# Kernel optimization log

Hardware: AMD Instinct MI355X
Metric: run time of the kernel (lower is better)

The kernel has to match this reference:

```python
import jax, jax.numpy as jnp
import numpy as np

HIDDEN = 1024
HEADS = 16
HEAD = HIDDEN // HEADS


def setup_inputs() -> dict:
    key = jax.random.key(0)
    ks = jax.random.split(key, 10)
    B, T, N = 4, 1024, 1024
    x = jax.random.normal(ks[0], (B, T, HIDDEN), dtype=jnp.float32)
    encoder_feature = jax.random.normal(ks[1], (B, N, HIDDEN), dtype=jnp.float32)
    s = 1.0 / np.sqrt(HIDDEN)
    Wq = jax.random.normal(ks[2], (HIDDEN, HIDDEN), dtype=jnp.float32) * s
    bq = jax.random.normal(ks[3], (HIDDEN,), dtype=jnp.float32) * 0.02
    Wk = jax.random.normal(ks[4], (HIDDEN, HIDDEN), dtype=jnp.float32) * s
    bk = jax.random.normal(ks[5], (HIDDEN,), dtype=jnp.float32) * 0.02
    Wv = jax.random.normal(ks[6], (HIDDEN, HIDDEN), dtype=jnp.float32) * s
    bv = jax.random.normal(ks[7], (HIDDEN,), dtype=jnp.float32) * 0.02
    return {"x": x, "encoder_feature": encoder_feature,
            "Wq": Wq, "bq": bq, "Wk": Wk, "bk": bk, "Wv": Wv, "bv": bv}


def reference(x, encoder_feature, Wq, bq, Wk, bk, Wv, bv):
    B, T, _ = x.shape
    N = encoder_feature.shape[1]
    # torch Linear: y = x @ W.T + b
    q = (x @ Wq.T + bq).reshape(B, T, HEADS, HEAD)
    k = (encoder_feature @ Wk.T + bk).reshape(B, N, HEADS, HEAD)
    v = (encoder_feature @ Wv.T + bv).reshape(B, N, HEADS, HEAD)
    att = jnp.einsum('bthd,bnhd->bhtn', q, k) / jnp.sqrt(jnp.float32(HEAD))
    # causal tril mask sliced to (T, N): position t attends to n <= t
    mask = jnp.tril(jnp.ones((T, N), dtype=bool))
    att = jnp.where(mask[None, None], att, jnp.finfo(att.dtype).min)
    att = jax.nn.softmax(att, axis=-1)
    out = jnp.einsum('bhtn,bnhd->bthd', att, v).reshape(B, T, HIDDEN)
    # NOTE: original forward never applies out_proj; dropout=0.0 (identity)
    return out
```

## Files before the change

kernel.cpp:

```cpp
#include <hip/hip_runtime.h>
#include <hip/hip_bf16.h>
#include <cstdint>
#include <cstddef>

#define B_SZ 4
#define T_SZ 1024
#define N_SZ 1024
#define HID 1024
#define NHEADS 16
#define DHEAD 64

typedef __bf16 bf16x8 __attribute__((ext_vector_type(8)));
typedef __bf16 bf16x4 __attribute__((ext_vector_type(4)));
typedef float floatx4 __attribute__((ext_vector_type(4)));

#define LDT 72
#define LKV 72
#define LP  72

#define SM_SCALE_LOG2E 0.18033688011112042f

__device__ __forceinline__ void async_copy16(const void* gsrc, void* ldst) {
    __builtin_amdgcn_global_load_lds(
        (const __attribute__((address_space(1))) void*)(uintptr_t)gsrc,
        (__attribute__((address_space(3))) void*)(uintptr_t)ldst, 16, 0, 0);
}

__global__ __launch_bounds__(256)
void cvt5_f32_bf16(const float* __restrict__ x, const float* __restrict__ enc,
                   const float* __restrict__ wq, const float* __restrict__ wk,
                   const float* __restrict__ wv,
                   __bf16* __restrict__ xb, __bf16* __restrict__ eb,
                   __bf16* __restrict__ wqb, __bf16* __restrict__ wkb,
                   __bf16* __restrict__ wvb)
{
#pragma unroll
    for (int c = 0; c < 8; ++c) {
        const int chunk = blockIdx.x * 8 + c;
        const float* s; __bf16* d; int base;
        if (chunk < 2048)      { s = x;   d = xb;  base = chunk; }
        else if (chunk < 4096) { s = enc; d = eb;  base = chunk - 2048; }
        else if (chunk < 4608) { s = wq;  d = wqb; base = chunk - 4096; }
        else if (chunk < 5120) { s = wk;  d = wkb; base = chunk - 4608; }
        else                   { s = wv;  d = wvb; base = chunk - 5120; }
        const size_t off = (size_t)base * 2048 + (size_t)threadIdx.x * 8;
        const float4 a = *(const float4*)(s + off);
        const float4 b = *(const float4*)(s + off + 4);
        bf16x8 o;
        o[0] = (__bf16)a.x; o[1] = (__bf16)a.y; o[2] = (__bf16)a.z; o[3] = (__bf16)a.w;
        o[4] = (__bf16)b.x; o[5] = (__bf16)b.y; o[6] = (__bf16)b.z; o[7] = (__bf16)b.w;
        *(bf16x8*)(d + off) = o;
    }
}

#define PBAR() do {                              \
    asm volatile("" ::: "memory");               \
    __builtin_amdgcn_s_barrier();                \
    __builtin_amdgcn_sched_barrier(0);           \
} while (0)

#define MFMA_Q(QM, QN, BREG) do {                                             \
    __builtin_amdgcn_s_setprio(1);                                            \
    _Pragma("unroll")                                                         \
    for (int mf_ = 0; mf_ < 4; ++mf_) {                                       \
        _Pragma("unroll")                                                     \
        for (int nf_ = 0; nf_ < 2; ++nf_) {                                   \
            acc[QM][QN][mf_][nf_] = __builtin_amdgcn_mfma_f32_16x16x32_bf16(  \
                a[mf_][0], BREG[nf_][0], acc[QM][QN][mf_][nf_], 0, 0, 0);     \
            acc[QM][QN][mf_][nf_] = __builtin_amdgcn_mfma_f32_16x16x32_bf16(  \
                a[mf_][1], BREG[nf_][1], acc[QM][QN][mf_][nf_], 0, 0, 0);     \
        }                                                                     \
    }                                                                         \
    __builtin_amdgcn_s_setprio(0);                                            \
} while (0)

#define LOAD_A(BUF, HALF) do {                                                \
    _Pragma("unroll")                                                         \
    for (int mf_ = 0; mf_ < 4; ++mf_) {                                       \
        a[mf_][0] = ldsA(BUF, HALF, mf_, 0);                                  \
        a[mf_][1] = ldsA(BUF, HALF, mf_, 1);                                  \
    }                                                                         \
} while (0)

#define LOAD_B(DST, BUF, HALF) do {                                           \
    _Pragma("unroll")                                                         \
    for (int nf_ = 0; nf_ < 2; ++nf_) {                                       \
        DST[nf_][0] = ldsB(BUF, HALF, nf_, 0);                                \
        DST[nf_][1] = ldsB(BUF, HALF, nf_, 1);                                \
    }                                                                         \
} while (0)

__global__ __launch_bounds__(512, 2)
void gemm3_256_8ph(const __bf16* __restrict__ xb, const __bf16* __restrict__ eb,
                   const __bf16* __restrict__ wqb, const __bf16* __restrict__ wkb,
                   const __bf16* __restrict__ wvb,
                   const float* __restrict__ bq, const float* __restrict__ bk,
                   const float* __restrict__ bv,
                   __bf16* __restrict__ qo, __bf16* __restrict__ ko,
                   __bf16* __restrict__ vo)
{
    __shared__ __align__(16) __bf16 AS[2][2][8192];
    __shared__ __align__(16) __bf16 BS[2][2][8192];

    const int bid = blockIdx.x;
    const int swz = (bid & 7) * 24 + (bid >> 3);
    const int mt  = swz >> 2;
    const int nt  = swz & 3;
    const int z   = mt >> 4;
    const int bm  = (mt & 15) << 8;
    const int bn  = nt << 8;

    const __bf16* A; const __bf16* W; const float* bias; __bf16* C;
    if (z == 0)      { A = xb; W = wqb; bias = bq; C = qo; }
    else if (z == 1) { A = eb; W = wkb; bias = bk; C = ko; }
    else             { A = eb; W = wvb; bias = bv; C = vo; }

    const int tid  = threadIdx.x;
    const int lane = tid & 63;
    const int wid  = tid >> 6;
    const int l15  = lane & 15;
    const int quad = lane >> 4;
    const int wmid = wid >> 2;
    const int wnid = wid & 3;

    const int sr  = tid >> 3;
    const int sch = tid & 7;

    auto stage2 = [&](const __bf16* src, __bf16* dst, int gRow0, int kt) {
        const int c = (sch ^ (sr & 7)) << 3;
        async_copy16(src + (size_t)(gRow0 + sr) * HID + kt * 64 + c,
                     (char*)dst + tid * 16);
        async_copy16(src + (size_t)(gRow0 + sr + 64) * HID + kt * 64 + c,
                     (char*)dst + 8192 + tid * 16);
    };

    auto ldsA = [&](int buf, int half, int mf, int kk) -> bf16x8 {
        const int r = wmid * 64 + mf * 16 + l15;
        return *(const bf16x8*)((const char*)&AS[buf][half][0] + r * 128 +
                                (((kk * 4 + quad) ^ (r & 7)) << 4));
    };
    auto ldsB = [&](int buf, int half, int nf, int kk) -> bf16x8 {
        const int r = wnid * 32 + nf * 16 + l15;
        return *(const bf16x8*)((const char*)&BS[buf][half][0] + r * 128 +
                                (((kk * 4 + quad) ^ (r & 7)) << 4));
    };

    bf16x8 a[4][2], b0[2][2], b1[2][2];
    floatx4 acc[2][2][4][2];
#pragma unroll
    for (int i = 0; i < 2; ++i)
#pragma unroll
        for (int j = 0; j < 2; ++j)
#pragma unroll
            for (int m = 0; m < 4; ++m)
#pragma unroll
                for (int n = 0; n < 2; ++n)
                    acc[i][j][m][n] = (floatx4)(0.0f);

    stage2(A, &AS[0][0][0], bm,       0);
    stage2(W, &BS[0][0][0], bn,       0);
    stage2(W, &BS[0][1][0], bn + 128, 0);
    stage2(A, &AS[0][1][0], bm + 128, 0);
    stage2(A, &AS[1][0][0], bm,       1);
    stage2(W, &BS[1][0][0], bn,       1);
    stage2(W, &BS[1][1][0], bn + 128, 1);
    asm volatile("s_waitcnt vmcnt(6)" ::: "memory");
    PBAR();

#pragma unroll 1
    for (int it = 0; it < 8; ++it) {
        const int kt1 = 2 * it + 1;
        const int kta = (it < 7) ? 2 * it + 2 : 14;
        const int ktb = (it < 7) ? 2 * it + 3 : 15;

        LOAD_A(0, 0);
        LOAD_B(b0, 0, 0);
        stage2(A, &AS[1][1][0], bm + 128, kt1);
        PBAR();
        MFMA_Q(0, 0, b0);
        PBAR();
        LOAD_B(b1, 0, 1);
        stage2(A, &AS[0][0][0], bm, kta);
        PBAR();
        MFMA_Q(0, 1, b1);
        PBAR();
        LOAD_A(0, 1);
        stage2(W, &BS[0][0][0], bn, kta);
        PBAR();
        MFMA_Q(1, 1, b1);
        PBAR();
        stage2(W, &BS[0][1][0], bn + 128, kta);
        PBAR();
        MFMA_Q(1, 0, b0);
        asm volatile("s_waitcnt vmcnt(6)" ::: "memory");
        PBAR();
        LOAD_A(1, 0);
        LOAD_B(b0, 1, 0);
        stage2(A, &AS[0][1][0], bm + 128, kta);
        PBAR();
        MFMA_Q(0, 0, b0);
        PBAR();
        LOAD_B(b1, 1, 1);
        stage2(A, &AS[1][0][0], bm, ktb);
        PBAR();
        MFMA_Q(0, 1, b1);
        PBAR();
        LOAD_A(1, 1);
        stage2(W, &BS[1][0][0], bn, ktb);
        PBAR();
        MFMA_Q(1, 1, b1);
        PBAR();
        stage2(W, &BS[1][1][0], bn + 128, ktb);
        PBAR();
        MFMA_Q(1, 0, b0);
        asm volatile("s_waitcnt vmcnt(6)" ::: "memory");
        PBAR();
    }

#pragma unroll
    for (int qn = 0; qn < 2; ++qn)
#pragma unroll
        for (int nf = 0; nf < 2; ++nf) {
            const int n = bn + qn * 128 + wnid * 32 + nf * 16 + l15;
            const float bias_f = bias[n];
#pragma unroll
            for (int qm = 0; qm < 2; ++qm)
#pragma unroll
                for (int mf = 0; mf < 4; ++mf) {
                    const int m0 = bm + qm * 128 + wmid * 64 + mf * 16 + quad * 4;
#pragma unroll
                    for (int r = 0; r < 4; ++r)
                        C[(size_t)(m0 + r) * HID + n] =
                            (__bf16)(acc[qm][qn][mf][nf][r] + bias_f);
                }
        }
}

#undef LOAD_A
#undef LOAD_B
#undef MFMA_Q
#undef PBAR

__global__ __launch_bounds__(256)
void gemm_bt_bias_f32in(const float* __restrict__ A,
                        const float* __restrict__ W,
                        const float* __restrict__ bias,
                        __hip_bfloat16* __restrict__ C)
{
    constexpr int K = HID;
    __shared__ __align__(16) __hip_bfloat16 As[128 * LDT];
    __shared__ __align__(16) __hip_bfloat16 Bs[128 * LDT];

    const int tid  = threadIdx.x;
    const int wave = tid >> 6;
    const int lane = tid & 63;
    const int bm = blockIdx.y * 128;
    const int bn = blockIdx.x * 128;
    const int wm = (wave >> 1) * 64;
    const int wn = (wave & 1) * 64;

    floatx4 acc[4][4];
#pragma unroll
    for (int i = 0; i < 4; ++i)
#pragma unroll
        for (int j = 0; j < 4; ++j)
            acc[i][j] = (floatx4)(0.0f);

    const int lr = tid >> 4;
    const int lc = (tid & 15) * 4;

    for (int k0 = 0; k0 < K; k0 += 64) {
#pragma unroll
        for (int qq = 0; qq < 8; ++qq) {
            const int r = lr + qq * 16;
            const float4 a4 = *(const float4*)(A + (size_t)(bm + r) * K + k0 + lc);
            const float4 w4 = *(const float4*)(W + (size_t)(bn + r) * K + k0 + lc);
            bf16x4 av, wv;
            av[0] = (__bf16)a4.x; av[1] = (__bf16)a4.y; av[2] = (__bf16)a4.z; av[3] = (__bf16)a4.w;
            wv[0] = (__bf16)w4.x; wv[1] = (__bf16)w4.y; wv[2] = (__bf16)w4.z; wv[3] = (__bf16)w4.w;
            *(bf16x4*)(As + r * LDT + lc) = av;
            *(bf16x4*)(Bs + r * LDT + lc) = wv;
        }
        __syncthreads();
#pragma unroll
        for (int kk = 0; kk < 2; ++kk) {
            const int krow = kk * 32 + (lane >> 4) * 8;
            const int mrow = wm + (lane & 15);
            const int nrow = wn + (lane & 15);
            bf16x8 af[4], bfr[4];
#pragma unroll
            for (int i = 0; i < 4; ++i) {
                af[i]  = *(const bf16x8*)(As + (mrow + i * 16) * LDT + krow);
                bfr[i] = *(const bf16x8*)(Bs + (nrow + i * 16) * LDT + krow);
            }
#pragma unroll
            for (int mi = 0; mi < 4; ++mi)
#pragma unroll
                for (int ni = 0; ni < 4; ++ni)
                    acc[mi][ni] = __builtin_amdgcn_mfma_f32_16x16x32_bf16(
                        af[mi], bfr[ni], acc[mi][ni], 0, 0, 0);
        }
        __syncthreads();
    }

    const int crow0 = bm + wm + (lane >> 4) * 4;
    const int ccol0 = bn + wn + (lane & 15);
#pragma unroll
    for (int ni = 0; ni < 4; ++ni) {
        const int n = ccol0 + ni * 16;
        const float bias_f = bias[n];
#pragma unroll
        for (int mi = 0; mi < 4; ++mi) {
#pragma unroll
            for (int r = 0; r < 4; ++r) {
                const int m = crow0 + mi * 16 + r;
                C[(size_t)m * HID + n] = __float2bfloat16(acc[mi][ni][r] + bias_f);
            }
        }
    }
}

__global__ __launch_bounds__(256)
void attn_flash_mfma_v4(const __bf16* __restrict__ q,
                        const __bf16* __restrict__ k,
                        const __bf16* __restrict__ v,
                        float* __restrict__ out)
{
    __shared__ __align__(16) __bf16 Ks[2][64 * LKV];
    __shared__ __align__(16) __bf16 Vt[2][64 * LKV];
    __shared__ __align__(16) __bf16 Ps[4][32 * LP];

    const int tid  = threadIdx.x;
    const int wave = tid >> 6;
    const int lane = tid & 63;
    const int l15  = lane & 15;
    const int quad = lane >> 4;

    const int bx = blockIdx.x;
    const int jj = bx & 7;
    const int bt = ((bx >> 8) & 1) ? jj : 7 - jj;
    const int bh = bx >> 3;
    const int h  = bh & (NHEADS - 1);
    const int b  = bh >> 4;
    const int t0 = bt * 128;

    const __bf16* kbase = k + (size_t)b * N_SZ * HID + h * DHEAD;
    const __bf16* vbase = v + (size_t)b * N_SZ * HID + h * DHEAD;

    bf16x8 qf[2][2];
    {
        const __bf16* qb = q + (size_t)(b * T_SZ + t0 + wave * 32) * HID + h * DHEAD;
#pragma unroll
        for (int g = 0; g < 2; ++g)
#pragma unroll
            for (int kk = 0; kk < 2; ++kk) {
                const bf16x8 raw = *(const bf16x8*)(qb + (size_t)(g * 16 + l15) * HID
                                                    + kk * 32 + quad * 8);
#pragma unroll
                for (int j = 0; j < 8; ++j)
                    qf[g][kk][j] = (__bf16)((float)raw[j] * SM_SCALE_LOG2E);
            }
    }

    const int kr = tid >> 3;
    const int kc = (tid & 7) * 8;
    const int vn = tid & 63;
    const int vd = (tid >> 6) * 8;

#pragma unroll
    for (int p = 0; p < 2; ++p) {
        *(bf16x8*)(&Ks[0][(kr + p * 32) * LKV + kc]) =
            *(const bf16x8*)(kbase + (size_t)(kr + p * 32) * HID + kc);
        const bf16x8 vv = *(const bf16x8*)(vbase + (size_t)vn * HID + vd + p * 32);
#pragma unroll
        for (int j = 0; j < 8; ++j)
            Vt[0][(vd + p * 32 + j) * LKV + vn] = vv[j];
    }
    __syncthreads();

    float lsum[2] = {0.f, 0.f};
    floatx4 oacc[2][4];
#pragma unroll
    for (int g = 0; g < 2; ++g)
#pragma unroll
        for (int nd = 0; nd < 4; ++nd) oacc[g][nd] = (floatx4)(0.0f);

    __bf16* pw = &Ps[wave][0];
    const int ntiles = 2 * bt + 2;

    for (int it = 0; it < ntiles; ++it) {
        const int bi = it & 1;
        const int n0 = it * 64;

        bf16x8 nk0, nk1, nv0, nv1;
        const bool pf = (it + 1 < ntiles);
        if (pf) {
            const int nn0 = n0 + 64;
            nk0 = *(const bf16x8*)(kbase + (size_t)(nn0 + kr) * HID + kc);
            nk1 = *(const bf16x8*)(kbase + (size_t)(nn0 + kr + 32) * HID + kc);
            nv0 = *(const bf16x8*)(vbase + (size_t)(nn0 + vn) * HID + vd);
            nv1 = *(const bf16x8*)(vbase + (size_t)(nn0 + vn) * HID + vd + 32);
        }

        floatx4 st[2][4];
#pragma unroll
        for (int g = 0; g < 2; ++g)
#pragma unroll
            for (int ni = 0; ni < 4; ++ni) st[g][ni] = (floatx4)(0.0f);
        const __bf16* ksb = &Ks[bi][0];
#pragma unroll
        for (int kk = 0; kk < 2; ++kk) {
            const int ko = kk * 32 + quad * 8;
#pragma unroll
            for (int ni = 0; ni < 4; ++ni) {
                const bf16x8 af = *(const bf16x8*)(ksb + (ni * 16 + l15) * LKV + ko);
                st[0][ni] = __builtin_amdgcn_mfma_f32_16x16x32_bf16(af, qf[0][kk], st[0][ni], 0, 0, 0);
                st[1][ni] = __builtin_amdgcn_mfma_f32_16x16x32_bf16(af, qf[1][kk], st[1][ni], 0, 0, 0);
            }
        }

        const bool msk = (it >= 2 * bt);
#pragma unroll
        for (int g = 0; g < 2; ++g) {
            const int tq = t0 + wave * 32 + g * 16 + l15;
#pragma unroll
            for (int ni = 0; ni < 4; ++ni) {
                bf16x4 pk;
#pragma unroll
                for (int r = 0; r < 4; ++r) {
                    float p = exp2f(st[g][ni][r]);
                    if (msk) {
                        const int nn = n0 + ni * 16 + quad * 4 + r;
                        p = (nn > tq) ? 0.f : p;
                    }
                    lsum[g] += p;
                    pk[r] = (__bf16)p;
                }
                *(bf16x4*)(pw + (g * 16 + l15) * LP + ni * 16 + quad * 4) = pk;
            }
        }

        const __bf16* vtb = &Vt[bi][0];
#pragma unroll
        for (int kk = 0; kk < 2; ++kk) {
            const int ko = kk * 32 + quad * 8;
            const bf16x8 bp0 = *(const bf16x8*)(pw + l15 * LP + ko);
            const bf16x8 bp1 = *(const bf16x8*)(pw + (16 + l15) * LP + ko);
#pragma unroll
            for (int nd = 0; nd < 4; ++nd) {
                const bf16x8 av = *(const bf16x8*)(vtb + (nd * 16 + l15) * LKV + ko);
                oacc[0][nd] = __builtin_amdgcn_mfma_f32_16x16x32_bf16(av, bp0, oacc[0][nd], 0, 0, 0);
                oacc[1][nd] = __builtin_amdgcn_mfma_f32_16x16x32_bf16(av, bp1, oacc[1][nd], 0, 0, 0);
            }
        }

        if (pf) {
            const int wb = bi ^ 1;
            *(bf16x8*)(&Ks[wb][kr * LKV + kc]) = nk0;
            *(bf16x8*)(&Ks[wb][(kr + 32) * LKV + kc]) = nk1;
#pragma unroll
            for (int j = 0; j < 8; ++j) {
                Vt[wb][(vd + j) * LKV + vn] = nv0[j];
                Vt[wb][(vd + 32 + j) * LKV + vn] = nv1[j];
            }
        }
        __syncthreads();
    }

#pragma unroll
    for (int g = 0; g < 2; ++g) {
        lsum[g] += __shfl_xor(lsum[g], 16, 64);
        lsum[g] += __shfl_xor(lsum[g], 32, 64);
    }
#pragma unroll
    for (int g = 0; g < 2; ++g) {
        const float invl = 1.0f / lsum[g];
        const int trow = t0 + wave * 32 + g * 16 + l15;
        float* ob = out + (size_t)(b * T_SZ + trow) * HID + h * DHEAD + quad * 4;
#pragma unroll
        for (int nd = 0; nd < 4; ++nd) {
            float4 o4;
            o4.x = oacc[g][nd][0] * invl;
            o4.y = oacc[g][nd][1] * invl;
            o4.z = oacc[g][nd][2] * invl;
            o4.w = oacc[g][nd][3] * invl;
            *(float4*)(ob + nd * 16) = o4;
        }
    }
}

extern "C" void kernel_launch(void* const* d_in, const int* in_sizes, int n_in,
                              void* d_out, int out_size, void* d_ws, size_t ws_size,
                              hipStream_t stream) {
    const float* x   = (const float*)d_in[0];
    const float* enc = (const float*)d_in[1];
    const float* Wq  = (const float*)d_in[2];
    const float* bq  = (const float*)d_in[3];
    const float* Wk  = (const float*)d_in[4];
    const float* bk  = (const float*)d_in[5];
    const float* Wv  = (const float*)d_in[6];
    const float* bv  = (const float*)d_in[7];
    float* out = (float*)d_out;

    char* ws = (char*)d_ws;
    const size_t MiB = 1024 * 1024;
    __bf16* q_ws = (__bf16*)(ws);
    __bf16* k_ws = (__bf16*)(ws + 8 * MiB);
    __bf16* v_ws = (__bf16*)(ws + 16 * MiB);

    const dim3 blk(256);
    if (ws_size >= 46 * MiB) {
        __bf16* xb  = (__bf16*)(ws + 24 * MiB);
        __bf16* eb  = (__bf16*)(ws + 32 * MiB);
        __bf16* wqb = (__bf16*)(ws + 40 * MiB);
        __bf16* wkb = (__bf16*)(ws + 42 * MiB);
        __bf16* wvb = (__bf16*)(ws + 44 * MiB);
        cvt5_f32_bf16<<<dim3(704), blk, 0, stream>>>(x, enc, Wq, Wk, Wv,
                                                     xb, eb, wqb, wkb, wvb);
        gemm3_256_8ph<<<dim3(192), dim3(512), 0, stream>>>(
            xb, eb, wqb, wkb, wvb, bq, bk, bv, q_ws, k_ws, v_ws);
    } else {
        const dim3 gg(HID / 128, (B_SZ * T_SZ) / 128);
        gemm_bt_bias_f32in<<<gg, blk, 0, stream>>>(x,   Wq, bq, (__hip_bfloat16*)q_ws);
        gemm_bt_bias_f32in<<<gg, blk, 0, stream>>>(enc, Wk, bk, (__hip_bfloat16*)k_ws);
        gemm_bt_bias_f32in<<<gg, blk, 0, stream>>>(enc, Wv, bv, (__hip_bfloat16*)v_ws);
    }

    attn_flash_mfma_v4<<<dim3(512), blk, 0, stream>>>(q_ws, k_ws, v_ws, out);
}
```

Measured before the change: 160.8 us.

## Halve attention query tile, swizzle LDS layouts, add MFMA priority hints

```diff
diff --git a/kernel.cpp b/kernel.cpp
--- a/kernel.cpp
+++ b/kernel.cpp
@@ -12,13 +12,14 @@
 
 typedef __bf16 bf16x8 __attribute__((ext_vector_type(8)));
 typedef __bf16 bf16x4 __attribute__((ext_vector_type(4)));
+typedef __bf16 bf16x2 __attribute__((ext_vector_type(2)));
 typedef float floatx4 __attribute__((ext_vector_type(4)));
 
 #define LDT 72
-#define LKV 72
-#define LP  72
 
 #define SM_SCALE_LOG2E 0.18033688011112042f
+
+#define SWZ(row, colbyte) (((row) << 7) + ((((colbyte) + (((row) & 7) << 4))) & 127))
 
 __device__ __forceinline__ void async_copy16(const void* gsrc, void* ldst) {
     __builtin_amdgcn_global_load_lds(
@@ -320,15 +321,15 @@
     }
 }
 
-__global__ __launch_bounds__(256)
-void attn_flash_mfma_v4(const __bf16* __restrict__ q,
+__global__ __launch_bounds__(256, 4)
+void attn_flash_mfma_v5(const __bf16* __restrict__ q,
                         const __bf16* __restrict__ k,
                         const __bf16* __restrict__ v,
                         float* __restrict__ out)
 {
-    __shared__ __align__(16) __bf16 Ks[2][64 * LKV];
-    __shared__ __align__(16) __bf16 Vt[2][64 * LKV];
-    __shared__ __align__(16) __bf16 Ps[4][32 * LP];
+    __shared__ __align__(16) char Ks[2][64 * 128];
+    __shared__ __align__(16) char Vt[2][64 * 128];
+    __shared__ __align__(16) char Ps[4][16 * 128];
 
     const int tid  = threadIdx.x;
     const int wave = tid >> 6;
@@ -337,153 +338,144 @@
     const int quad = lane >> 4;
 
     const int bx = blockIdx.x;
-    const int jj = bx & 7;
-    const int bt = ((bx >> 8) & 1) ? jj : 7 - jj;
-    const int bh = bx >> 3;
+    const int jj = bx & 15;
+    const int bt = ((bx >> 8) & 1) ? jj : 15 - jj;
+    const int bh = bx >> 4;
     const int h  = bh & (NHEADS - 1);
     const int b  = bh >> 4;
-    const int t0 = bt * 128;
+    const int t0 = bt * 64;
 
     const __bf16* kbase = k + (size_t)b * N_SZ * HID + h * DHEAD;
     const __bf16* vbase = v + (size_t)b * N_SZ * HID + h * DHEAD;
 
-    bf16x8 qf[2][2];
+    bf16x8 qf[2];
     {
-        const __bf16* qb = q + (size_t)(b * T_SZ + t0 + wave * 32) * HID + h * DHEAD;
-#pragma unroll
-        for (int g = 0; g < 2; ++g)
-#pragma unroll
-            for (int kk = 0; kk < 2; ++kk) {
-                const bf16x8 raw = *(const bf16x8*)(qb + (size_t)(g * 16 + l15) * HID
-                                                    + kk * 32 + quad * 8);
-#pragma unroll
-                for (int j = 0; j < 8; ++j)
-                    qf[g][kk][j] = (__bf16)((float)raw[j] * SM_SCALE_LOG2E);
-            }
-    }
-
-    const int kr = tid >> 3;
-    const int kc = (tid & 7) * 8;
-    const int vn = tid & 63;
-    const int vd = (tid >> 6) * 8;
-
-#pragma unroll
-    for (int p = 0; p < 2; ++p) {
-        *(bf16x8*)(&Ks[0][(kr + p * 32) * LKV + kc]) =
-            *(const bf16x8*)(kbase + (size_t)(kr + p * 32) * HID + kc);
-        const bf16x8 vv = *(const bf16x8*)(vbase + (size_t)vn * HID + vd + p * 32);
-#pragma unroll
-        for (int j = 0; j < 8; ++j)
-            Vt[0][(vd + p * 32 + j) * LKV + vn] = vv[j];
+        const __bf16* qb = q + (size_t)(b * T_SZ + t0 + wave * 16 + l15) * HID + h * DHEAD;
+#pragma unroll
+        for (int kk = 0; kk < 2; ++kk) {
+            const bf16x8 raw = *(const bf16x8*)(qb + kk * 32 + quad * 8);
+#pragma unroll
+            for (int j = 0; j < 8; ++j)
+                qf[kk][j] = (__bf16)((float)raw[j] * SM_SCALE_LOG2E);
+        }
+    }
+
+    const int kr  = tid >> 3;
+    const int kce = (tid & 7) * 8;
+    const int vn2 = (tid & 31) * 2;
+    const int vd2 = (tid >> 5) * 8;
+
+    {
+        *(bf16x8*)(&Ks[0][0] + SWZ(kr, kce * 2)) =
+            *(const bf16x8*)(kbase + (size_t)kr * HID + kce);
+        *(bf16x8*)(&Ks[0][0] + SWZ(kr + 32, kce * 2)) =
+            *(const bf16x8*)(kbase + (size_t)(kr + 32) * HID + kce);
+        const bf16x8 va = *(const bf16x8*)(vbase + (size_t)vn2 * HID + vd2);
+        const bf16x8 vb = *(const bf16x8*)(vbase + (size_t)(vn2 + 1) * HID + vd2);
+#pragma unroll
+        for (int j = 0; j < 8; ++j) {
+            bf16x2 t2; t2[0] = va[j]; t2[1] = vb[j];
+            *(bf16x2*)(&Vt[0][0] + SWZ(vd2 + j, vn2 * 2)) = t2;
+        }
     }
     __syncthreads();
 
-    float lsum[2] = {0.f, 0.f};
-    floatx4 oacc[2][4];
-#pragma unroll
-    for (int g = 0; g < 2; ++g)
-#pragma unroll
-        for (int nd = 0; nd < 4; ++nd) oacc[g][nd] = (floatx4)(0.0f);
-
-    __bf16* pw = &Ps[wave][0];
-    const int ntiles = 2 * bt + 2;
+    float lsum = 0.f;
+    floatx4 oacc[4];
+#pragma unroll
+    for (int nd = 0; nd < 4; ++nd) oacc[nd] = (floatx4)(0.0f);
+
+    char* pw = &Ps[wave][0];
+    const int ntiles = bt + 1;
+    const int tq = t0 + wave * 16 + l15;
 
     for (int it = 0; it < ntiles; ++it) {
         const int bi = it & 1;
         const int n0 = it * 64;
 
-        bf16x8 nk0, nk1, nv0, nv1;
+        bf16x8 nk0, nk1, nva, nvb;
         const bool pf = (it + 1 < ntiles);
         if (pf) {
             const int nn0 = n0 + 64;
-            nk0 = *(const bf16x8*)(kbase + (size_t)(nn0 + kr) * HID + kc);
-            nk1 = *(const bf16x8*)(kbase + (size_t)(nn0 + kr + 32) * HID + kc);
-            nv0 = *(const bf16x8*)(vbase + (size_t)(nn0 + vn) * HID + vd);
-            nv1 = *(const bf16x8*)(vbase + (size_t)(nn0 + vn) * HID + vd + 32);
-        }
-
-        floatx4 st[2][4];
-#pragma unroll
-        for (int g = 0; g < 2; ++g)
-#pragma unroll
-            for (int ni = 0; ni < 4; ++ni) st[g][ni] = (floatx4)(0.0f);
-        const __bf16* ksb = &Ks[bi][0];
+            nk0 = *(const bf16x8*)(kbase + (size_t)(nn0 + kr) * HID + kce);
+            nk1 = *(const bf16x8*)(kbase + (size_t)(nn0 + kr + 32) * HID + kce);
+            nva = *(const bf16x8*)(vbase + (size_t)(nn0 + vn2) * HID + vd2);
+            nvb = *(const bf16x8*)(vbase + (size_t)(nn0 + vn2 + 1) * HID + vd2);
+        }
+
+        floatx4 st[4];
+#pragma unroll
+        for (int ni = 0; ni < 4; ++ni) st[ni] = (floatx4)(0.0f);
+        const char* ksb = &Ks[bi][0];
+        __builtin_amdgcn_s_setprio(1);
 #pragma unroll
         for (int kk = 0; kk < 2; ++kk) {
-            const int ko = kk * 32 + quad * 8;
+            const int cb = kk * 64 + quad * 16;
 #pragma unroll
             for (int ni = 0; ni < 4; ++ni) {
-                const bf16x8 af = *(const bf16x8*)(ksb + (ni * 16 + l15) * LKV + ko);
-                st[0][ni] = __builtin_amdgcn_mfma_f32_16x16x32_bf16(af, qf[0][kk], st[0][ni], 0, 0, 0);
-                st[1][ni] = __builtin_amdgcn_mfma_f32_16x16x32_bf16(af, qf[1][kk], st[1][ni], 0, 0, 0);
+                const bf16x8 af = *(const bf16x8*)(ksb + SWZ(ni * 16 + l15, cb));
+                st[ni] = __builtin_amdgcn_mfma_f32_16x16x32_bf16(af, qf[kk], st[ni], 0, 0, 0);
             }
         }
-
-        const bool msk = (it >= 2 * bt);
-#pragma unroll
-        for (int g = 0; g < 2; ++g) {
-            const int tq = t0 + wave * 32 + g * 16 + l15;
-#pragma unroll
-            for (int ni = 0; ni < 4; ++ni) {
-                bf16x4 pk;
-#pragma unroll
-                for (int r = 0; r < 4; ++r) {
-                    float p = exp2f(st[g][ni][r]);
-                    if (msk) {
-                        const int nn = n0 + ni * 16 + quad * 4 + r;
-                        p = (nn > tq) ? 0.f : p;
-                    }
-                    lsum[g] += p;
-                    pk[r] = (__bf16)p;
+        __builtin_amdgcn_s_setprio(0);
+
+        const bool msk = (it == bt);
+#pragma unroll
+        for (int ni = 0; ni < 4; ++ni) {
+            bf16x4 pk;
+#pragma unroll
+            for (int r = 0; r < 4; ++r) {
+                float p = exp2f(st[ni][r]);
+                if (msk) {
+                    const int nn = n0 + ni * 16 + quad * 4 + r;
+                    p = (nn > tq) ? 0.f : p;
                 }
-                *(bf16x4*)(pw + (g * 16 + l15) * LP + ni * 16 + quad * 4) = pk;
+                lsum += p;
+                pk[r] = (__bf16)p;
             }
-        }
-
-        const __bf16* vtb = &Vt[bi][0];
+            *(bf16x4*)(pw + SWZ(l15, ni * 32 + quad * 8)) = pk;
+        }
+
+        const char* vtb = &Vt[bi][0];
+        __builtin_amdgcn_s_setprio(1);
 #pragma unroll
         for (int kk = 0; kk < 2; ++kk) {
-            const int ko = kk * 32 + quad * 8;
-            const bf16x8 bp0 = *(const bf16x8*)(pw + l15 * LP + ko);
-            const bf16x8 bp1 = *(const bf16x8*)(pw + (16 + l15) * LP + ko);
+            const int cb = kk * 64 + quad * 16;
+            const bf16x8 bp = *(const bf16x8*)(pw + SWZ(l15, cb));
 #pragma unroll
             for (int nd = 0; nd < 4; ++nd) {
-                const bf16x8 av = *(const bf16x8*)(vtb + (nd * 16 + l15) * LKV + ko);
-                oacc[0][nd] = __builtin_amdgcn_mfma_f32_16x16x32_bf16(av, bp0, oacc[0][nd], 0, 0, 0);
-                oacc[1][nd] = __builtin_amdgcn_mfma_f32_16x16x32_bf16(av, bp1, oacc[1][nd], 0, 0, 0);
+                const bf16x8 av = *(const bf16x8*)(vtb + SWZ(nd * 16 + l15, cb));
+                oacc[nd] = __builtin_amdgcn_mfma_f32_16x16x32_bf16(av, bp, oacc[nd], 0, 0, 0);
             }
         }
+        __builtin_amdgcn_s_setprio(0);
 
         if (pf) {
-            const int wb = bi ^ 1;
-            *(bf16x8*)(&Ks[wb][kr * LKV + kc]) = nk0;
-            *(bf16x8*)(&Ks[wb][(kr + 32) * LKV + kc]) = nk1;
+            char* kd = &Ks[bi ^ 1][0];
+            char* vd = &Vt[bi ^ 1][0];
+            *(bf16x8*)(kd + SWZ(kr, kce * 2)) = nk0;
+            *(bf16x8*)(kd + SWZ(kr + 32, kce * 2)) = nk1;
 #pragma unroll
             for (int j = 0; j < 8; ++j) {
-                Vt[wb][(vd + j) * LKV + vn] = nv0[j];
-                Vt[wb][(vd + 32 + j) * LKV + vn] = nv1[j];
+                bf16x2 t2; t2[0] = nva[j]; t2[1] = nvb[j];
+                *(bf16x2*)(vd + SWZ(vd2 + j, vn2 * 2)) = t2;
             }
         }
         __syncthreads();
     }
 
-#pragma unroll
-    for (int g = 0; g < 2; ++g) {
-        lsum[g] += __shfl_xor(lsum[g], 16, 64);
-        lsum[g] += __shfl_xor(lsum[g], 32, 64);
-    }
-#pragma unroll
-    for (int g = 0; g < 2; ++g) {
-        const float invl = 1.0f / lsum[g];
-        const int trow = t0 + wave * 32 + g * 16 + l15;
-        float* ob = out + (size_t)(b * T_SZ + trow) * HID + h * DHEAD + quad * 4;
+    lsum += __shfl_xor(lsum, 16, 64);
+    lsum += __shfl_xor(lsum, 32, 64);
+    {
+        const float invl = 1.0f / lsum;
+        float* ob = out + (size_t)(b * T_SZ + tq) * HID + h * DHEAD + quad * 4;
 #pragma unroll
         for (int nd = 0; nd < 4; ++nd) {
             float4 o4;
-            o4.x = oacc[g][nd][0] * invl;
-            o4.y = oacc[g][nd][1] * invl;
-            o4.z = oacc[g][nd][2] * invl;
-            o4.w = oacc[g][nd][3] * invl;
+            o4.x = oacc[nd][0] * invl;
+            o4.y = oacc[nd][1] * invl;
+            o4.z = oacc[nd][2] * invl;
+            o4.w = oacc[nd][3] * invl;
             *(float4*)(ob + nd * 16) = o4;
         }
     }
@@ -526,5 +518,5 @@
         gemm_bt_bias_f32in<<<gg, blk, 0, stream>>>(enc, Wv, bv, (__hip_bfloat16*)v_ws);
     }
 
-    attn_flash_mfma_v4<<<dim3(512), blk, 0, stream>>>(q_ws, k_ws, v_ws, out);
+    attn_flash_mfma_v5<<<dim3(1024), blk, 0, stream>>>(q_ws, k_ws, v_ws, out);
 }
```

Measured after the change: 154.1 us. 4.2% less time.
